# Kernel tuning notes

Hardware: AMD Instinct MI355X
Metric: run time of the kernel (lower is better)

## Reference

```python
import jax, jax.numpy as jnp
import numpy as np

N_NODES = 100000
N_EDGES = 1600000
IN_FEAT = 256
HIDDEN = 64
N_CLASSES = 16


def gcn_conv(x, edge_index, W, b):
    """PyG GCNConv: add self-loops, symmetric normalization, linear+aggregate."""
    n = x.shape[0]
    src, dst = edge_index[0], edge_index[1]
    loops = jnp.arange(n, dtype=src.dtype)
    src = jnp.concatenate([src, loops])
    dst = jnp.concatenate([dst, loops])
    # in-degree on graph with self-loops
    deg = jax.ops.segment_sum(jnp.ones(src.shape[0], dtype=x.dtype), dst, num_segments=n)
    dinv = jnp.where(deg > 0, jax.lax.rsqrt(deg), 0.0)
    h = x @ W                                  # [N, out]
    norm = dinv[src] * dinv[dst]               # [E+N]
    msg = h[src] * norm[:, None]                # gather + scale (memory-bound)
    out = jax.ops.segment_sum(msg, dst, num_segments=n)  # scatter-add
    return out + b


def setup_inputs() -> dict:
    key = jax.random.key(0)
    ks = jax.random.split(key, 5)
    x = jax.random.normal(ks[0], (N_NODES, IN_FEAT), dtype=jnp.float32)
    edge_index = jax.random.randint(ks[1], (2, N_EDGES), 0, N_NODES, dtype=jnp.int64)
    W1 = jax.random.normal(ks[2], (IN_FEAT, HIDDEN), dtype=jnp.float32) * (1.0 / np.sqrt(IN_FEAT))
    b1 = jnp.zeros((HIDDEN,), dtype=jnp.float32)
    W2 = jax.random.normal(ks[3], (HIDDEN, N_CLASSES), dtype=jnp.float32) * (1.0 / np.sqrt(HIDDEN))
    b2 = jnp.zeros((N_CLASSES,), dtype=jnp.float32)
    return {"x": x, "edge_index": edge_index, "W1": W1, "b1": b1, "W2": W2, "b2": b2}


def reference(x, edge_index, W1, b1, W2, b2):
    h = gcn_conv(x, edge_index, W1, b1)
    h = jax.nn.relu(h)
    # dropout p=0.5 is identity in eval mode (training=False)
    out = gcn_conv(h, edge_index, W2, b2)
    return out
```

## Files before the change

kernel.cpp:

```cpp
#include <hip/hip_runtime.h>

#define NN 100000
#define NE 1600000
#define FIN 256
#define FH 64
#define FC 16

#define SCAN_CHUNK 1024
#define NB_SCAN ((NN + SCAN_CHUNK - 1) / SCAN_CHUNK)
#define NSWEEP 2
#define SWEEP_W ((NN + NSWEEP - 1) / NSWEEP)
#define NB_COUNT ((NE + 255) / 256)
#define NB_GEMM1 ((NN + 63) / 64)

typedef int v2i __attribute__((ext_vector_type(2)));

__global__ void detect_k(const int* __restrict__ ei, int* __restrict__ flag) {
    if (threadIdx.x == 0 && blockIdx.x == 0) {
        int z = (ei[1] == 0) & (ei[3] == 0) & (ei[5] == 0) & (ei[7] == 0);
        *flag = z;
    }
}

__device__ __forceinline__ int eidx(const int* __restrict__ ei, int f, int pos) {
    return f ? ei[2 * pos] : ei[pos];
}

__global__ __launch_bounds__(256, 8) void fused_k(const int* __restrict__ ei,
                                                  const int* __restrict__ flag,
                                                  int* __restrict__ deg,
                                                  v2i* __restrict__ packed,
                                                  const float* __restrict__ x,
                                                  const float* __restrict__ W,
                                                  float* __restrict__ h) {
    __shared__ float As[32][68];
    __shared__ float Bs[32][64];
    if (blockIdx.x < NB_COUNT) {
        int e = blockIdx.x * 256 + threadIdx.x;
        if (e >= NE) return;
        int f = *flag;
        int s = eidx(ei, f, e);
        int d = eidx(ei, f, NE + e);
        int r = atomicAdd(&deg[d], 1);
        v2i p; p.x = s; p.y = d | (r << 17);
        packed[e] = p;
        return;
    }
    const int t = threadIdx.x;
    const int r0 = (blockIdx.x - NB_COUNT) * 64;
    const int tx4 = (t & 15) * 4;
    const int ty4 = (t >> 4) * 4;
    const int xkf = (t & 7) * 4;
    const int xrow = t >> 3;
    const int wcol = (t & 15) * 4;
    const int wrow = t >> 4;

    float acc[4][4] = {};

    for (int k0 = 0; k0 < FIN; k0 += 32) {
        #pragma unroll
        for (int i = 0; i < 2; i++) {
            int row = xrow + 32 * i;
            int gr = r0 + row;
            float4 v = make_float4(0.f, 0.f, 0.f, 0.f);
            if (gr < NN) v = *(const float4*)&x[gr * FIN + k0 + xkf];
            As[xkf + 0][row] = v.x;
            As[xkf + 1][row] = v.y;
            As[xkf + 2][row] = v.z;
            As[xkf + 3][row] = v.w;
            int kr = wrow + 16 * i;
            float4 w = *(const float4*)&W[(k0 + kr) * FH + wcol];
            *(float4*)&Bs[kr][wcol] = w;
        }
        __syncthreads();
        #pragma unroll 8
        for (int kk = 0; kk < 32; kk++) {
            float4 a = *(const float4*)&As[kk][ty4];
            float4 b = *(const float4*)&Bs[kk][tx4];
            float av[4] = {a.x, a.y, a.z, a.w};
            float bv[4] = {b.x, b.y, b.z, b.w};
            #pragma unroll
            for (int i2 = 0; i2 < 4; i2++)
                #pragma unroll
                for (int j2 = 0; j2 < 4; j2++)
                    acc[i2][j2] = fmaf(av[i2], bv[j2], acc[i2][j2]);
        }
        __syncthreads();
    }
    #pragma unroll
    for (int i2 = 0; i2 < 4; i2++) {
        int r = r0 + ty4 + i2;
        if (r < NN)
            *(float4*)&h[r * FH + tx4] =
                make_float4(acc[i2][0], acc[i2][1], acc[i2][2], acc[i2][3]);
    }
}

__global__ __launch_bounds__(256) void scan_sum_k(const int* __restrict__ deg,
                                                  int* __restrict__ partial,
                                                  float* __restrict__ dinv) {
    __shared__ int red[256];
    int b = blockIdx.x, t = threadIdx.x;
    int base = b * SCAN_CHUNK + t * 4;
    int s = 0;
    #pragma unroll
    for (int i = 0; i < 4; i++) {
        int idx = base + i;
        if (idx < NN) {
            int dv = deg[idx];
            s += dv;
            dinv[idx] = rsqrtf((float)(dv + 1));
        }
    }
    red[t] = s;
    __syncthreads();
    for (int off = 128; off > 0; off >>= 1) {
        if (t < off) red[t] += red[t + off];
        __syncthreads();
    }
    if (t == 0) partial[b] = red[0];
}

__global__ __launch_bounds__(128) void scan_part_k(int* __restrict__ partial) {
    __shared__ int s[128];
    int t = threadIdx.x;
    int v = (t < NB_SCAN) ? partial[t] : 0;
    s[t] = v; __syncthreads();
    for (int off = 1; off < 128; off <<= 1) {
        int u = (t >= off) ? s[t - off] : 0;
        __syncthreads();
        s[t] += u;
        __syncthreads();
    }
    if (t < NB_SCAN) partial[t] = s[t] - v;
}

__global__ __launch_bounds__(256) void scan_out_k(const int* __restrict__ deg,
                                                  const int* __restrict__ partial,
                                                  int* __restrict__ row_start) {
    __shared__ int s[256];
    int b = blockIdx.x, t = threadIdx.x;
    int base = b * SCAN_CHUNK + t * 4;
    int v[4]; int sum = 0;
    #pragma unroll
    for (int i = 0; i < 4; i++) {
        int idx = base + i;
        v[i] = (idx < NN) ? deg[idx] : 0;
        sum += v[i];
    }
    s[t] = sum; __syncthreads();
    for (int off = 1; off < 256; off <<= 1) {
        int u = (t >= off) ? s[t - off] : 0;
        __syncthreads();
        s[t] += u;
        __syncthreads();
    }
    int run = partial[b] + s[t] - sum;
    #pragma unroll
    for (int i = 0; i < 4; i++) {
        int idx = base + i;
        if (idx < NN) {
            row_start[idx] = run;
            run += v[i];
            if (idx == NN - 1) row_start[NN] = run;
        }
    }
}

__global__ __launch_bounds__(256) void fill_k(const v2i* __restrict__ packed,
                                              const int* __restrict__ row_start,
                                              int* __restrict__ csr,
                                              int lo, int hi) {
    int e = blockIdx.x * 256 + threadIdx.x;
    if (e >= NE) return;
    v2i p = __builtin_nontemporal_load(&packed[e]);
    int d = p.y & 0x1FFFF;
    if (d < lo || d >= hi) return;
    int r = ((unsigned)p.y) >> 17;
    csr[row_start[d] + r] = p.x;
}

__global__ __launch_bounds__(256) void agg1g_k(const int* __restrict__ csr,
                                               const int* __restrict__ row_start,
                                               const float* __restrict__ h1,
                                               const float* __restrict__ dinv,
                                               const float* __restrict__ b1,
                                               const float* __restrict__ W2,
                                               float* __restrict__ h2) {
    __shared__ float sW2[FH * FC];
    __shared__ float sp[4][FH];
    const int t = threadIdx.x;
    #pragma unroll
    for (int i = 0; i < 4; i++) sW2[t + 256 * i] = W2[t + 256 * i];
    __syncthreads();

    int wid = t >> 6;
    int n = blockIdx.x * 4 + wid;
    int lane = t & 63;
    if (n >= NN) return;
    int s0 = row_start[n], s1 = row_start[n + 1];
    float acc = 0.f, a0 = 0.f, a1 = 0.f, a2 = 0.f, a3 = 0.f;
    for (int j0 = s0; j0 < s1; j0 += 64) {
        int idx = j0 + lane;
        int sl = 0; float wl = 0.f;
        if (idx < s1) { sl = csr[idx]; wl = dinv[sl]; }
        int cnt = s1 - j0; if (cnt > 64) cnt = 64;
        int j = 0;
        for (; j + 4 <= cnt; j += 4) {
            int   sA = __shfl(sl, j + 0, 64), sB = __shfl(sl, j + 1, 64);
            int   sC = __shfl(sl, j + 2, 64), sD = __shfl(sl, j + 3, 64);
            float wA = __shfl(wl, j + 0, 64), wB = __shfl(wl, j + 1, 64);
            float wC = __shfl(wl, j + 2, 64), wD = __shfl(wl, j + 3, 64);
            float hA = h1[sA * FH + lane];
            float hB = h1[sB * FH + lane];
            float hC = h1[sC * FH + lane];
            float hD = h1[sD * FH + lane];
            a0 = fmaf(hA, wA, a0); a1 = fmaf(hB, wB, a1);
            a2 = fmaf(hC, wC, a2); a3 = fmaf(hD, wD, a3);
        }
        for (; j < cnt; j++) {
            int   s = __shfl(sl, j, 64);
            float w = __shfl(wl, j, 64);
            acc = fmaf(h1[s * FH + lane], w, acc);
        }
    }
    acc += (a0 + a1) + (a2 + a3);
    float dn = dinv[n];
    acc = fmaf(h1[n * FH + lane], dn, acc);
    float p = fmaf(acc, dn, b1[lane]);
    sp[wid][lane] = fmaxf(p, 0.f);
    __builtin_amdgcn_s_waitcnt(0);
    if (lane < FC) {
        float o = 0.f;
        #pragma unroll 8
        for (int k = 0; k < FH; k++)
            o = fmaf(sp[wid][k], sW2[k * FC + lane], o);
        h2[n * FC + lane] = o;
    }
}

__global__ __launch_bounds__(256) void agg2_k(const int* __restrict__ csr,
                                              const int* __restrict__ row_start,
                                              const float* __restrict__ h2,
                                              const float* __restrict__ dinv,
                                              const float* __restrict__ b2,
                                              float* __restrict__ out) {
    int n = blockIdx.x * 16 + (threadIdx.x >> 4);
    int l16 = threadIdx.x & 15;
    int base = threadIdx.x & 48;
    if (n >= NN) return;
    int s0 = row_start[n], s1 = row_start[n + 1];
    float acc = 0.f, a0 = 0.f, a1 = 0.f, a2 = 0.f, a3 = 0.f;
    for (int j0 = s0; j0 < s1; j0 += 16) {
        int idx = j0 + l16;
        int sl = 0; float wl = 0.f;
        if (idx < s1) { sl = csr[idx]; wl = dinv[sl]; }
        int cnt = s1 - j0; if (cnt > 16) cnt = 16;
        int j = 0;
        for (; j + 4 <= cnt; j += 4) {
            int   sA = __shfl(sl, base + j + 0, 64), sB = __shfl(sl, base + j + 1, 64);
            int   sC = __shfl(sl, base + j + 2, 64), sD = __shfl(sl, base + j + 3, 64);
            float wA = __shfl(wl, base + j + 0, 64), wB = __shfl(wl, base + j + 1, 64);
            float wC = __shfl(wl, base + j + 2, 64), wD = __shfl(wl, base + j + 3, 64);
            float hA = h2[sA * FC + l16];
            float hB = h2[sB * FC + l16];
            float hC = h2[sC * FC + l16];
            float hD = h2[sD * FC + l16];
            a0 = fmaf(hA, wA, a0); a1 = fmaf(hB, wB, a1);
            a2 = fmaf(hC, wC, a2); a3 = fmaf(hD, wD, a3);
        }
        for (; j < cnt; j++) {
            int   s = __shfl(sl, base + j, 64);
            float w = __shfl(wl, base + j, 64);
            acc = fmaf(h2[s * FC + l16], w, acc);
        }
    }
    acc += (a0 + a1) + (a2 + a3);
    float dn = dinv[n];
    acc = fmaf(h2[n * FC + l16], dn, acc);
    out[n * FC + l16] = fmaf(acc, dn, b2[l16]);
}

extern "C" void kernel_launch(void* const* d_in, const int* in_sizes, int n_in,
                              void* d_out, int out_size, void* d_ws, size_t ws_size,
                              hipStream_t stream) {
    const float* x  = (const float*)d_in[0];
    const int*   ei = (const int*)d_in[1];
    const float* W1 = (const float*)d_in[2];
    const float* b1 = (const float*)d_in[3];
    const float* W2 = (const float*)d_in[4];
    const float* b2 = (const float*)d_in[5];
    float* out = (float*)d_out;

    char* ws = (char*)d_ws;
    int*   deg       = (int*)(ws + 0);
    int*   row_start = (int*)(ws + 512 * 1024);
    float* dinv      = (float*)(ws + 1024 * 1024);
    int*   flag      = (int*)(ws + 1536 * 1024);
    int*   partial   = (int*)(ws + 1540 * 1024);
    int*   csr       = (int*)(ws + 2ull * 1024 * 1024);
    float* h1        = (float*)(ws + 9ull * 1024 * 1024);
    v2i*   packed    = (v2i*)(ws + 35ull * 1024 * 1024);
    float* h2        = (float*)(ws + 35ull * 1024 * 1024);

    detect_k<<<1, 64, 0, stream>>>(ei, flag);
    (void)hipMemsetAsync(deg, 0, NN * sizeof(int), stream);
    fused_k<<<NB_COUNT + NB_GEMM1, 256, 0, stream>>>(ei, flag, deg, packed, x, W1, h1);
    scan_sum_k<<<NB_SCAN, 256, 0, stream>>>(deg, partial, dinv);
    scan_part_k<<<1, 128, 0, stream>>>(partial);
    scan_out_k<<<NB_SCAN, 256, 0, stream>>>(deg, partial, row_start);
    for (int sw = 0; sw < NSWEEP; sw++)
        fill_k<<<(NE + 255) / 256, 256, 0, stream>>>(packed, row_start, csr,
                                                     sw * SWEEP_W, (sw + 1) * SWEEP_W);

    agg1g_k<<<(NN + 3) / 4, 256, 0, stream>>>(csr, row_start, h1, dinv, b1, W2, h2);
    agg2_k<<<(NN + 15) / 16, 256, 0, stream>>>(csr, row_start, h2, dinv, b2, out);
}
```

Before: 396.3 us.

## Interleave count and GEMM blocks; vectorize neighbor gathers with float4 subgroups

The fused count/GEMM kernel now interleaves its block types four count blocks per GEMM block, so the atomic degree counting runs alongside the compute-bound GEMM instead of before it. Both aggregation kernels switch from one float per lane per edge to float4 loads, with each subgroup of lanes handling a different edge. Partial sums are then combined across subgroups with xor shuffles. This is meant to cut the number of load instructions and increase memory-level parallelism in the gathers, at the cost of extra shuffle reductions and more complex tail handling.

After: 361.9 us. 8.7% less time.

```diff
diff --git a/kernel.cpp b/kernel.cpp
--- a/kernel.cpp
+++ b/kernel.cpp
@@ -12,8 +12,20 @@
 #define SWEEP_W ((NN + NSWEEP - 1) / NSWEEP)
 #define NB_COUNT ((NE + 255) / 256)
 #define NB_GEMM1 ((NN + 63) / 64)
+#define NB_FUSED (5 * NB_GEMM1)
 
 typedef int v2i __attribute__((ext_vector_type(2)));
+
+__device__ __forceinline__ float4 fma4(float4 v, float w, float4 a) {
+    a.x = fmaf(v.x, w, a.x); a.y = fmaf(v.y, w, a.y);
+    a.z = fmaf(v.z, w, a.z); a.w = fmaf(v.w, w, a.w);
+    return a;
+}
+__device__ __forceinline__ float4 xor_add4(float4 r, int m) {
+    r.x += __shfl_xor(r.x, m, 64); r.y += __shfl_xor(r.y, m, 64);
+    r.z += __shfl_xor(r.z, m, 64); r.w += __shfl_xor(r.w, m, 64);
+    return r;
+}
 
 __global__ void detect_k(const int* __restrict__ ei, int* __restrict__ flag) {
     if (threadIdx.x == 0 && blockIdx.x == 0) {
@@ -35,8 +47,11 @@
                                                   float* __restrict__ h) {
     __shared__ float As[32][68];
     __shared__ float Bs[32][64];
-    if (blockIdx.x < NB_COUNT) {
-        int e = blockIdx.x * 256 + threadIdx.x;
+    const int b = blockIdx.x;
+    if ((b % 5) != 4) {
+        int cb = (b / 5) * 4 + (b % 5);
+        if (cb >= NB_COUNT) return;
+        int e = cb * 256 + threadIdx.x;
         if (e >= NE) return;
         int f = *flag;
         int s = eidx(ei, f, e);
@@ -47,7 +62,7 @@
         return;
     }
     const int t = threadIdx.x;
-    const int r0 = (blockIdx.x - NB_COUNT) * 64;
+    const int r0 = (b / 5) * 64;
     const int tx4 = (t & 15) * 4;
     const int ty4 = (t >> 4) * 4;
     const int xkf = (t & 7) * 4;
@@ -76,9 +91,9 @@
         #pragma unroll 8
         for (int kk = 0; kk < 32; kk++) {
             float4 a = *(const float4*)&As[kk][ty4];
-            float4 b = *(const float4*)&Bs[kk][tx4];
+            float4 bq = *(const float4*)&Bs[kk][tx4];
             float av[4] = {a.x, a.y, a.z, a.w};
-            float bv[4] = {b.x, b.y, b.z, b.w};
+            float bv[4] = {bq.x, bq.y, bq.z, bq.w};
             #pragma unroll
             for (int i2 = 0; i2 < 4; i2++)
                 #pragma unroll
@@ -198,37 +213,58 @@
     int n = blockIdx.x * 4 + wid;
     int lane = t & 63;
     if (n >= NN) return;
+    int sg = lane >> 4;
+    int fl = lane & 15;
     int s0 = row_start[n], s1 = row_start[n + 1];
-    float acc = 0.f, a0 = 0.f, a1 = 0.f, a2 = 0.f, a3 = 0.f;
+    float4 A = make_float4(0.f, 0.f, 0.f, 0.f);
+    float4 B = make_float4(0.f, 0.f, 0.f, 0.f);
     for (int j0 = s0; j0 < s1; j0 += 64) {
         int idx = j0 + lane;
         int sl = 0; float wl = 0.f;
         if (idx < s1) { sl = csr[idx]; wl = dinv[sl]; }
         int cnt = s1 - j0; if (cnt > 64) cnt = 64;
         int j = 0;
-        for (; j + 4 <= cnt; j += 4) {
-            int   sA = __shfl(sl, j + 0, 64), sB = __shfl(sl, j + 1, 64);
-            int   sC = __shfl(sl, j + 2, 64), sD = __shfl(sl, j + 3, 64);
-            float wA = __shfl(wl, j + 0, 64), wB = __shfl(wl, j + 1, 64);
-            float wC = __shfl(wl, j + 2, 64), wD = __shfl(wl, j + 3, 64);
-            float hA = h1[sA * FH + lane];
-            float hB = h1[sB * FH + lane];
-            float hC = h1[sC * FH + lane];
-            float hD = h1[sD * FH + lane];
-            a0 = fmaf(hA, wA, a0); a1 = fmaf(hB, wB, a1);
-            a2 = fmaf(hC, wC, a2); a3 = fmaf(hD, wD, a3);
-        }
-        for (; j < cnt; j++) {
-            int   s = __shfl(sl, j, 64);
-            float w = __shfl(wl, j, 64);
-            acc = fmaf(h1[s * FH + lane], w, acc);
-        }
-    }
-    acc += (a0 + a1) + (a2 + a3);
-    float dn = dinv[n];
-    acc = fmaf(h1[n * FH + lane], dn, acc);
-    float p = fmaf(acc, dn, b1[lane]);
-    sp[wid][lane] = fmaxf(p, 0.f);
+        for (; j + 8 <= cnt; j += 8) {
+            int   eA = __shfl(sl, j + sg, 64);
+            float wA = __shfl(wl, j + sg, 64);
+            int   eB = __shfl(sl, j + 4 + sg, 64);
+            float wB = __shfl(wl, j + 4 + sg, 64);
+            float4 vA = *(const float4*)&h1[eA * FH + fl * 4];
+            float4 vB = *(const float4*)&h1[eB * FH + fl * 4];
+            A = fma4(vA, wA, A);
+            B = fma4(vB, wB, B);
+        }
+        if (j + 4 <= cnt) {
+            int   eA = __shfl(sl, j + sg, 64);
+            float wA = __shfl(wl, j + sg, 64);
+            float4 vA = *(const float4*)&h1[eA * FH + fl * 4];
+            A = fma4(vA, wA, A);
+            j += 4;
+        }
+        int rem = cnt - j;
+        if (rem > 0) {
+            int jj = j + (sg < rem ? sg : 0);
+            int   eA = __shfl(sl, jj, 64);
+            float wA = __shfl(wl, jj, 64);
+            if (sg >= rem) wA = 0.f;
+            float4 vA = *(const float4*)&h1[eA * FH + fl * 4];
+            A = fma4(vA, wA, A);
+        }
+    }
+    float4 r = make_float4(A.x + B.x, A.y + B.y, A.z + B.z, A.w + B.w);
+    r = xor_add4(r, 16);
+    r = xor_add4(r, 32);
+    if (sg == 0) {
+        float dn = dinv[n];
+        float4 self = *(const float4*)&h1[n * FH + fl * 4];
+        float4 bq = *(const float4*)&b1[fl * 4];
+        float4 p;
+        p.x = fmaxf(fmaf(fmaf(self.x, dn, r.x), dn, bq.x), 0.f);
+        p.y = fmaxf(fmaf(fmaf(self.y, dn, r.y), dn, bq.y), 0.f);
+        p.z = fmaxf(fmaf(fmaf(self.z, dn, r.z), dn, bq.z), 0.f);
+        p.w = fmaxf(fmaf(fmaf(self.w, dn, r.w), dn, bq.w), 0.f);
+        *(float4*)&sp[wid][fl * 4] = p;
+    }
     __builtin_amdgcn_s_waitcnt(0);
     if (lane < FC) {
         float o = 0.f;
@@ -245,40 +281,63 @@
                                               const float* __restrict__ dinv,
                                               const float* __restrict__ b2,
                                               float* __restrict__ out) {
-    int n = blockIdx.x * 16 + (threadIdx.x >> 4);
-    int l16 = threadIdx.x & 15;
-    int base = threadIdx.x & 48;
+    const int t = threadIdx.x;
+    int n = blockIdx.x * 16 + (t >> 4);
+    int l16 = t & 15;
+    int base = t & 48;
+    int q = (t >> 2) & 3;
+    int c = t & 3;
     if (n >= NN) return;
     int s0 = row_start[n], s1 = row_start[n + 1];
-    float acc = 0.f, a0 = 0.f, a1 = 0.f, a2 = 0.f, a3 = 0.f;
+    float4 A = make_float4(0.f, 0.f, 0.f, 0.f);
+    float4 B = make_float4(0.f, 0.f, 0.f, 0.f);
     for (int j0 = s0; j0 < s1; j0 += 16) {
         int idx = j0 + l16;
         int sl = 0; float wl = 0.f;
         if (idx < s1) { sl = csr[idx]; wl = dinv[sl]; }
         int cnt = s1 - j0; if (cnt > 16) cnt = 16;
         int j = 0;
-        for (; j + 4 <= cnt; j += 4) {
-            int   sA = __shfl(sl, base + j + 0, 64), sB = __shfl(sl, base + j + 1, 64);
-            int   sC = __shfl(sl, base + j + 2, 64), sD = __shfl(sl, base + j + 3, 64);
-            float wA = __shfl(wl, base + j + 0, 64), wB = __shfl(wl, base + j + 1, 64);
-            float wC = __shfl(wl, base + j + 2, 64), wD = __shfl(wl, base + j + 3, 64);
-            float hA = h2[sA * FC + l16];
-            float hB = h2[sB * FC + l16];
-            float hC = h2[sC * FC + l16];
-            float hD = h2[sD * FC + l16];
-            a0 = fmaf(hA, wA, a0); a1 = fmaf(hB, wB, a1);
-            a2 = fmaf(hC, wC, a2); a3 = fmaf(hD, wD, a3);
-        }
-        for (; j < cnt; j++) {
-            int   s = __shfl(sl, base + j, 64);
-            float w = __shfl(wl, base + j, 64);
-            acc = fmaf(h2[s * FC + l16], w, acc);
-        }
-    }
-    acc += (a0 + a1) + (a2 + a3);
-    float dn = dinv[n];
-    acc = fmaf(h2[n * FC + l16], dn, acc);
-    out[n * FC + l16] = fmaf(acc, dn, b2[l16]);
+        for (; j + 8 <= cnt; j += 8) {
+            int   eA = __shfl(sl, base + j + q, 64);
+            float wA = __shfl(wl, base + j + q, 64);
+            int   eB = __shfl(sl, base + j + 4 + q, 64);
+            float wB = __shfl(wl, base + j + 4 + q, 64);
+            float4 vA = *(const float4*)&h2[eA * FC + c * 4];
+            float4 vB = *(const float4*)&h2[eB * FC + c * 4];
+            A = fma4(vA, wA, A);
+            B = fma4(vB, wB, B);
+        }
+        if (j + 4 <= cnt) {
+            int   eA = __shfl(sl, base + j + q, 64);
+            float wA = __shfl(wl, base + j + q, 64);
+            float4 vA = *(const float4*)&h2[eA * FC + c * 4];
+            A = fma4(vA, wA, A);
+            j += 4;
+        }
+        int rem = cnt - j;
+        if (rem > 0) {
+            int jj = base + j + (q < rem ? q : 0);
+            int   eA = __shfl(sl, jj, 64);
+            float wA = __shfl(wl, jj, 64);
+            if (q >= rem) wA = 0.f;
+            float4 vA = *(const float4*)&h2[eA * FC + c * 4];
+            A = fma4(vA, wA, A);
+        }
+    }
+    float4 r = make_float4(A.x + B.x, A.y + B.y, A.z + B.z, A.w + B.w);
+    r = xor_add4(r, 4);
+    r = xor_add4(r, 8);
+    if (q == 0) {
+        float dn = dinv[n];
+        float4 self = *(const float4*)&h2[n * FC + c * 4];
+        float4 bq = *(const float4*)&b2[c * 4];
+        float4 p;
+        p.x = fmaf(fmaf(self.x, dn, r.x), dn, bq.x);
+        p.y = fmaf(fmaf(self.y, dn, r.y), dn, bq.y);
+        p.z = fmaf(fmaf(self.z, dn, r.z), dn, bq.z);
+        p.w = fmaf(fmaf(self.w, dn, r.w), dn, bq.w);
+        *(float4*)&out[n * FC + c * 4] = p;
+    }
 }
 
 extern "C" void kernel_launch(void* const* d_in, const int* in_sizes, int n_in,
@@ -305,7 +364,7 @@
 
     detect_k<<<1, 64, 0, stream>>>(ei, flag);
     (void)hipMemsetAsync(deg, 0, NN * sizeof(int), stream);
-    fused_k<<<NB_COUNT + NB_GEMM1, 256, 0, stream>>>(ei, flag, deg, packed, x, W1, h1);
+    fused_k<<<NB_FUSED, 256, 0, stream>>>(ei, flag, deg, packed, x, W1, h1);
     scan_sum_k<<<NB_SCAN, 256, 0, stream>>>(deg, partial, dinv);
     scan_part_k<<<1, 128, 0, stream>>>(partial);
     scan_out_k<<<NB_SCAN, 256, 0, stream>>>(deg, partial, row_start);
```
